# Kernel optimization log

Measured on AMD Instinct MI355X. Metric: run time of the kernel, lower is better.

## Reference

```python
import jax, jax.numpy as jnp
import numpy as np


def setup_inputs() -> dict:
    key = jax.random.key(0)
    k1, k2 = jax.random.split(key)
    BATCH, SLOTS = 64, 65536   # 64 ciphertexts, 2^16 CKKS slots each
    NUM_T = 16                 # number of BSGS diagonal transforms (shifts 2^0..2^15)
    x = jax.random.normal(k1, (BATCH, SLOTS), dtype=jnp.float32)
    diagonals = jax.random.normal(k2, (NUM_T, SLOTS), dtype=jnp.float32)
    return {"x": x, "diagonals": diagonals, "stride": 1, "reps": 1}


def reference(x, diagonals, stride, reps):
    """FHE BSGS conv-as-linear-transform: rotate / plaintext-multiply / accumulate.

    Mirrors LinearTransform.evaluate_transforms:
      for i: out += roll(x, -2**i * stride) * diagonals[i]
      (two rescales are scale-management no-ops numerically)
      final conv roll by slots // (2 * reps).
    """
    slots = x.shape[-1]
    num_t = diagonals.shape[0]
    # Vectorize the rotations: gather all shifted copies at once.
    # shift for transform i is -2**i * stride (roll left by 2**i*stride).
    shifts = (2 ** jnp.arange(num_t, dtype=jnp.int32)) * stride        # [T]
    base = jnp.arange(slots, dtype=jnp.int32)                          # [S]
    idx = (base[None, :] + shifts[:, None]) % slots                    # [T, S] roll(-s) gather
    rolled = x[:, idx]                                                 # [B, T, S]
    out = jnp.einsum('bts,ts->bs', rolled, diagonals)                  # accumulate products
    # final conv roll: roll(slots // (2*reps)) => shift right
    out = jnp.roll(out, slots // (2 * reps), axis=-1)
    return out
```

## Files before the change

### kernel.cpp

```cpp
#include <hip/hip_runtime.h>


#define SLOTS 65536
#define MASK  65535
#define NB    4
#define STRIPW 2048

__global__ __launch_bounds__(256) void bsgs_kernel(
    const float* __restrict__ x,
    const float* __restrict__ diag,
    float* __restrict__ out)
{
    __shared__ float sstrip[NB][STRIPW];

    const int bid  = blockIdx.x;
    const int y    = bid & 15;
    const int xidx = bid >> 4;
    const int tid  = threadIdx.x;
    const int J    = xidx * 1024;
    const int j    = J + tid * 4;
    const int bg   = y * NB;

    float4 dreg[16];
#pragma unroll
    for (int t = 0; t < 16; ++t)
        dreg[t] = *(const float4*)(diag + t * SLOTS + j);

#pragma unroll
    for (int b = 0; b < NB; ++b) {
        const float* __restrict__ xr = x + (size_t)(bg + b) * SLOTS;
#pragma unroll
        for (int h = 0; h < 2; ++h) {
            const int i = tid * 4 + h * 1024;
            *(float4*)(&sstrip[b][i]) = *(const float4*)(xr + ((J + i) & MASK));
        }
    }
    __syncthreads();

    float4 acc[NB];
#pragma unroll
    for (int b = 0; b < NB; ++b) acc[b] = make_float4(0.f, 0.f, 0.f, 0.f);

#pragma unroll
    for (int b = 0; b < NB; ++b) {
        const float* __restrict__ xr = x + (size_t)(bg + b) * SLOTS;

        float4 vd[5];
#pragma unroll
        for (int t = 11; t < 16; ++t)
            vd[t - 11] = *(const float4*)(xr + ((j + (1 << t)) & MASK));

        const float* sp = &sstrip[b][tid * 4];
        const float4 v0 = *(const float4*)(sp);
        const float4 w4 = *(const float4*)(sp + 4);

        acc[b].x += v0.y * dreg[0].x + v0.z * dreg[1].x;
        acc[b].y += v0.z * dreg[0].y + v0.w * dreg[1].y;
        acc[b].z += v0.w * dreg[0].z + w4.x * dreg[1].z;
        acc[b].w += w4.x * dreg[0].w + w4.y * dreg[1].w;

        acc[b].x += w4.x * dreg[2].x; acc[b].y += w4.y * dreg[2].y;
        acc[b].z += w4.z * dreg[2].z; acc[b].w += w4.w * dreg[2].w;

#pragma unroll
        for (int t = 3; t <= 10; ++t) {
            const float4 v = *(const float4*)(sp + (1 << t));
            acc[b].x += v.x * dreg[t].x; acc[b].y += v.y * dreg[t].y;
            acc[b].z += v.z * dreg[t].z; acc[b].w += v.w * dreg[t].w;
        }

#pragma unroll
        for (int t = 11; t < 16; ++t) {
            const float4 v = vd[t - 11];
            acc[b].x += v.x * dreg[t].x; acc[b].y += v.y * dreg[t].y;
            acc[b].z += v.z * dreg[t].z; acc[b].w += v.w * dreg[t].w;
        }
    }

#pragma unroll
    for (int b = 0; b < NB; ++b)
        *(float4*)(out + (size_t)(bg + b) * SLOTS + (j ^ 32768)) = acc[b];
}

extern "C" void kernel_launch(void* const* d_in, const int* in_sizes, int n_in,
                              void* d_out, int out_size, void* d_ws, size_t ws_size,
                              hipStream_t stream) {
    const float* x    = (const float*)d_in[0];
    const float* diag = (const float*)d_in[1];
    float* out        = (float*)d_out;

    bsgs_kernel<<<dim3(1024), dim3(256), 0, stream>>>(x, diag, out);
}
```

Before: 82.46 us.

## Stage diagonals in LDS, process 8 rows per 512-thread block, nontemporal stores

```diff
diff --git a/kernel.cpp b/kernel.cpp
--- a/kernel.cpp
+++ b/kernel.cpp
@@ -3,83 +3,108 @@
 
 #define SLOTS 65536
 #define MASK  65535
-#define NB    4
+#define NBR   8
+#define TILEW 1024
 #define STRIPW 2048
 
-__global__ __launch_bounds__(256) void bsgs_kernel(
+typedef __attribute__((ext_vector_type(4))) float f4v;
+
+__device__ __forceinline__ void ntstore4(float* p, const float4 v) {
+    f4v t = {v.x, v.y, v.z, v.w};
+    __builtin_nontemporal_store(t, (f4v*)p);
+}
+
+__global__ __launch_bounds__(512) void bsgs_kernel(
     const float* __restrict__ x,
     const float* __restrict__ diag,
     float* __restrict__ out)
 {
-    __shared__ float sstrip[NB][STRIPW];
+    __shared__ float  sstrip[NBR][STRIPW];
+    __shared__ float4 sdiag[16][TILEW / 4];
 
     const int bid  = blockIdx.x;
-    const int y    = bid & 15;
-    const int xidx = bid >> 4;
+    const int y    = bid & 7;
+    const int xidx = bid >> 3;
     const int tid  = threadIdx.x;
-    const int J    = xidx * 1024;
-    const int j    = J + tid * 4;
-    const int bg   = y * NB;
+    const int c4   = tid & 255;
+    const int rp   = tid >> 8;
+    const int J    = xidx * TILEW;
+    const int j    = J + c4 * 4;
+    const int bg   = y * NBR;
+    const int r0   = rp * 4;
 
-    float4 dreg[16];
+    float4 vd[4][5];
 #pragma unroll
-    for (int t = 0; t < 16; ++t)
-        dreg[t] = *(const float4*)(diag + t * SLOTS + j);
+    for (int q = 0; q < 4; ++q) {
+        const float* __restrict__ xr = x + (size_t)(bg + r0 + q) * SLOTS;
+#pragma unroll
+        for (int t = 11; t < 16; ++t)
+            vd[q][t - 11] = *(const float4*)(xr + ((j + (1 << t)) & MASK));
+    }
 
 #pragma unroll
-    for (int b = 0; b < NB; ++b) {
-        const float* __restrict__ xr = x + (size_t)(bg + b) * SLOTS;
+    for (int tt = 0; tt < 8; ++tt) {
+        const int t = tt * 2 + rp;
+        sdiag[t][c4] = *(const float4*)(diag + t * SLOTS + J + c4 * 4);
+    }
+
 #pragma unroll
-        for (int h = 0; h < 2; ++h) {
-            const int i = tid * 4 + h * 1024;
-            *(float4*)(&sstrip[b][i]) = *(const float4*)(xr + ((J + i) & MASK));
-        }
+    for (int r = 0; r < NBR; ++r) {
+        const float* __restrict__ xr = x + (size_t)(bg + r) * SLOTS;
+        *(float4*)(&sstrip[r][tid * 4]) =
+            *(const float4*)(xr + ((J + tid * 4) & MASK));
     }
     __syncthreads();
 
-    float4 acc[NB];
+    float4 acc[4];
 #pragma unroll
-    for (int b = 0; b < NB; ++b) acc[b] = make_float4(0.f, 0.f, 0.f, 0.f);
+    for (int q = 0; q < 4; ++q) acc[q] = make_float4(0.f, 0.f, 0.f, 0.f);
 
+    {
+        float4 v0[4], w4[4];
 #pragma unroll
-    for (int b = 0; b < NB; ++b) {
-        const float* __restrict__ xr = x + (size_t)(bg + b) * SLOTS;
-
-        float4 vd[5];
+        for (int q = 0; q < 4; ++q) {
+            const float* sp = &sstrip[r0 + q][c4 * 4];
+            v0[q] = *(const float4*)(sp);
+            w4[q] = *(const float4*)(sp + 4);
+        }
+        const float4 d0 = sdiag[0][c4];
+        const float4 d1 = sdiag[1][c4];
+        const float4 d2 = sdiag[2][c4];
 #pragma unroll
-        for (int t = 11; t < 16; ++t)
-            vd[t - 11] = *(const float4*)(xr + ((j + (1 << t)) & MASK));
-
-        const float* sp = &sstrip[b][tid * 4];
-        const float4 v0 = *(const float4*)(sp);
-        const float4 w4 = *(const float4*)(sp + 4);
-
-        acc[b].x += v0.y * dreg[0].x + v0.z * dreg[1].x;
-        acc[b].y += v0.z * dreg[0].y + v0.w * dreg[1].y;
-        acc[b].z += v0.w * dreg[0].z + w4.x * dreg[1].z;
-        acc[b].w += w4.x * dreg[0].w + w4.y * dreg[1].w;
-
-        acc[b].x += w4.x * dreg[2].x; acc[b].y += w4.y * dreg[2].y;
-        acc[b].z += w4.z * dreg[2].z; acc[b].w += w4.w * dreg[2].w;
-
-#pragma unroll
-        for (int t = 3; t <= 10; ++t) {
-            const float4 v = *(const float4*)(sp + (1 << t));
-            acc[b].x += v.x * dreg[t].x; acc[b].y += v.y * dreg[t].y;
-            acc[b].z += v.z * dreg[t].z; acc[b].w += v.w * dreg[t].w;
-        }
-
-#pragma unroll
-        for (int t = 11; t < 16; ++t) {
-            const float4 v = vd[t - 11];
-            acc[b].x += v.x * dreg[t].x; acc[b].y += v.y * dreg[t].y;
-            acc[b].z += v.z * dreg[t].z; acc[b].w += v.w * dreg[t].w;
+        for (int q = 0; q < 4; ++q) {
+            acc[q].x += v0[q].y * d0.x + v0[q].z * d1.x + w4[q].x * d2.x;
+            acc[q].y += v0[q].z * d0.y + v0[q].w * d1.y + w4[q].y * d2.y;
+            acc[q].z += v0[q].w * d0.z + w4[q].x * d1.z + w4[q].z * d2.z;
+            acc[q].w += w4[q].x * d0.w + w4[q].y * d1.w + w4[q].w * d2.w;
         }
     }
 
 #pragma unroll
-    for (int b = 0; b < NB; ++b)
-        *(float4*)(out + (size_t)(bg + b) * SLOTS + (j ^ 32768)) = acc[b];
+    for (int t = 3; t <= 10; ++t) {
+        const float4 d = sdiag[t][c4];
+#pragma unroll
+        for (int q = 0; q < 4; ++q) {
+            const float4 v = *(const float4*)(&sstrip[r0 + q][c4 * 4 + (1 << t)]);
+            acc[q].x += v.x * d.x; acc[q].y += v.y * d.y;
+            acc[q].z += v.z * d.z; acc[q].w += v.w * d.w;
+        }
+    }
+
+#pragma unroll
+    for (int t = 11; t < 16; ++t) {
+        const float4 d = sdiag[t][c4];
+#pragma unroll
+        for (int q = 0; q < 4; ++q) {
+            const float4 v = vd[q][t - 11];
+            acc[q].x += v.x * d.x; acc[q].y += v.y * d.y;
+            acc[q].z += v.z * d.z; acc[q].w += v.w * d.w;
+        }
+    }
+
+#pragma unroll
+    for (int q = 0; q < 4; ++q)
+        ntstore4(out + (size_t)(bg + r0 + q) * SLOTS + (j ^ 32768), acc[q]);
 }
 
 extern "C" void kernel_launch(void* const* d_in, const int* in_sizes, int n_in,
@@ -89,5 +114,5 @@
     const float* diag = (const float*)d_in[1];
     float* out        = (float*)d_out;
 
-    bsgs_kernel<<<dim3(1024), dim3(256), 0, stream>>>(x, diag, out);
+    bsgs_kernel<<<dim3(512), dim3(512), 0, stream>>>(x, diag, out);
 }
```

Result: slower. 86.05 us (+4.3%).
